# Kernel optimization log

Hardware: AMD Instinct MI355X
Metric: run time of the kernel (lower is better)

The kernel has to match this reference:

```python
import jax, jax.numpy as jnp
import numpy as np

D = 512
HEADS, DIM_HEAD, LANDMARKS, PINV_ITERS = 8, 64, 256, 6
CONV_K = 33  # residual depthwise conv kernel over sequence dim


def _ln(x, g, b, eps=1e-5):
    mu = x.mean(-1, keepdims=True)
    var = ((x - mu) ** 2).mean(-1, keepdims=True)
    return (x - mu) / jnp.sqrt(var + eps) * g + b


def _moe(x, gw, gb, f1w, f1b, l1g, l1b, f2w, f2b, l2g, l2b, k):
    # Dense grouped-expert evaluation (same math as per-token dispatch in torch source).
    scores = x @ gw + gb                               # [B,N,E]
    topk_s, topk_i = jax.lax.top_k(scores, k)          # [B,N,k]
    h = jnp.einsum('bnd,edh->benh', x, f1w) + f1b[None, :, None, :]
    h = jax.nn.relu(_ln(h, l1g[None, :, None, :], l1b[None, :, None, :]))
    o = jnp.einsum('benh,ehd->bend', h, f2w) + f2b[None, :, None, :]
    o = _ln(o, l2g[None, :, None, :], l2b[None, :, None, :])  # [B,E,N,D]
    o = jnp.take_along_axis(jnp.swapaxes(o, 1, 2), topk_i[..., None], axis=2)  # [B,N,k,D]
    w = jax.nn.softmax(topk_s, axis=-1)[..., None]
    return (w * o).sum(axis=2) + x


def _pinv(x, iters):
    # Moore-Penrose iterative pseudoinverse (lucidrains nystrom-attention)
    col = jnp.abs(x).sum(-1).max()
    row = jnp.abs(x).sum(-2).max()
    z = jnp.swapaxes(x, -1, -2) / (col * row)
    I = jnp.eye(x.shape[-1], dtype=x.dtype)
    for _ in range(iters):
        xz = x @ z
        z = 0.25 * z @ (13 * I - xz @ (15 * I - xz @ (7 * I - xz)))
    return z


def _nystrom(x, qkv_w, out_w, out_b, conv_w):
    b, n, _ = x.shape
    m, h, dh = LANDMARKS, HEADS, DIM_HEAD
    pad = (m - n % m) % m
    x = jnp.pad(x, ((0, 0), (pad, 0), (0, 0)))  # pad at FRONT, as in source
    npd = n + pad
    qkv = x @ qkv_w                              # [b, npd, 3*h*dh]
    q, k, v = [t.reshape(b, npd, h, dh).transpose(0, 2, 1, 3) for t in jnp.split(qkv, 3, axis=-1)]
    q = q * dh ** -0.5
    l = npd // m
    q_l = q.reshape(b, h, m, l, dh).mean(3)      # landmark means
    k_l = k.reshape(b, h, m, l, dh).mean(3)
    attn1 = jax.nn.softmax(jnp.einsum('bhid,bhjd->bhij', q, k_l), -1)    # [b,h,npd,m]
    attn2 = jax.nn.softmax(jnp.einsum('bhid,bhjd->bhij', q_l, k_l), -1)  # [b,h,m,m]
    attn3 = jax.nn.softmax(jnp.einsum('bhid,bhjd->bhij', q_l, k), -1)    # [b,h,m,npd]
    out = (attn1 @ _pinv(attn2, PINV_ITERS)) @ (attn3 @ v)               # [b,h,npd,dh]
    res = jax.lax.conv_general_dilated(
        v, conv_w, (1, 1), [(CONV_K // 2, CONV_K // 2), (0, 0)],
        dimension_numbers=('NCHW', 'OIHW', 'NCHW'), feature_group_count=h)
    out = out + res
    out = out.transpose(0, 2, 1, 3).reshape(b, npd, h * dh)
    out = out @ out_w + out_b
    return out[:, -n:]


def setup_inputs() -> dict:
    key = jax.random.key(0)
    ks = iter(jax.random.split(key, 64))
    def rn(shape, s=0.02):
        return jax.random.normal(next(ks), shape, jnp.float32) * s
    inp = {'features': jax.random.normal(next(ks), (4, 6000, D), jnp.float32)}
    inp['cls_token'] = rn((1, 1, D), 1e-6)
    def moe_params(pfx, E):
        inp[pfx + '_gate_w'] = rn((D, E)); inp[pfx + '_gate_b'] = jnp.zeros((E,), jnp.float32)
        inp[pfx + '_fc1_w'] = rn((E, D, D)); inp[pfx + '_fc1_b'] = jnp.zeros((E, D), jnp.float32)
        inp[pfx + '_ln1_g'] = jnp.ones((E, D), jnp.float32); inp[pfx + '_ln1_b'] = jnp.zeros((E, D), jnp.float32)
        inp[pfx + '_fc2_w'] = rn((E, D, D)); inp[pfx + '_fc2_b'] = jnp.zeros((E, D), jnp.float32)
        inp[pfx + '_ln2_g'] = jnp.ones((E, D), jnp.float32); inp[pfx + '_ln2_b'] = jnp.zeros((E, D), jnp.float32)
    moe_params('moe1', 2)
    moe_params('moe2', 4)
    def layer_params(pfx):
        inp[pfx + '_norm_g'] = jnp.ones((D,), jnp.float32); inp[pfx + '_norm_b'] = jnp.zeros((D,), jnp.float32)
        inp[pfx + '_qkv_w'] = rn((D, 3 * HEADS * DIM_HEAD))
        inp[pfx + '_out_w'] = rn((HEADS * DIM_HEAD, D)); inp[pfx + '_out_b'] = jnp.zeros((D,), jnp.float32)
        inp[pfx + '_conv_w'] = rn((HEADS, 1, CONV_K, 1))
    layer_params('l1')
    layer_params('l2')
    return inp


def reference(features, cls_token,
              moe1_gate_w, moe1_gate_b, moe1_fc1_w, moe1_fc1_b, moe1_ln1_g, moe1_ln1_b, moe1_fc2_w, moe1_fc2_b, moe1_ln2_g, moe1_ln2_b,
              moe2_gate_w, moe2_gate_b, moe2_fc1_w, moe2_fc1_b, moe2_ln1_g, moe2_ln1_b, moe2_fc2_w, moe2_fc2_b, moe2_ln2_g, moe2_ln2_b,
              l1_norm_g, l1_norm_b, l1_qkv_w, l1_out_w, l1_out_b, l1_conv_w,
              l2_norm_g, l2_norm_b, l2_qkv_w, l2_out_w, l2_out_b, l2_conv_w):
    B, N, _ = features.shape
    _H = int(np.ceil(np.sqrt(N)))
    add = _H * _H - N
    h = jnp.concatenate([features, features[:, :add]], axis=1)      # square pad by wrap
    h = jnp.concatenate([jnp.broadcast_to(cls_token, (B, 1, D)), h], axis=1)
    h = _moe(h, moe1_gate_w, moe1_gate_b, moe1_fc1_w, moe1_fc1_b, moe1_ln1_g, moe1_ln1_b, moe1_fc2_w, moe1_fc2_b, moe1_ln2_g, moe1_ln2_b, k=1)
    h = h + _nystrom(_ln(h, l1_norm_g, l1_norm_b), l1_qkv_w, l1_out_w, l1_out_b, l1_conv_w)
    h = _moe(h, moe2_gate_w, moe2_gate_b, moe2_fc1_w, moe2_fc1_b, moe2_ln1_g, moe2_ln1_b, moe2_fc2_w, moe2_fc2_b, moe2_ln2_g, moe2_ln2_b, k=2)
    h = h + _nystrom(_ln(h, l2_norm_g, l2_norm_b), l2_qkv_w, l2_out_w, l2_out_b, l2_conv_w)
    return (h[:, 0], h[:, 1:])
```

## Files before the change

kernel.cpp:

```cpp
#include <hip/hip_runtime.h>
#include <hip/hip_bf16.h>

constexpr int BATCH = 4;
constexpr int NTOK  = 6085;
constexpr int BN_TOK = BATCH * NTOK;
constexpr int NPD   = 6144;
constexpr int RPAD  = BATCH * NPD;
constexpr int DMODEL = 512;
constexpr int NH = 8, DH = 64;
constexpr int NBH = BATCH * NH;
constexpr int LGRP = NPD / 256;
constexpr int PAD_FRONT = 59;
constexpr int CONVK = 33;
constexpr int NCH = 8;
constexpr int LISTCAP = 24576;

typedef __attribute__((ext_vector_type(8))) short short8v;
typedef __attribute__((ext_vector_type(4))) float f32x4;

__device__ __forceinline__ unsigned short f2bf(float f) {
  unsigned u = __float_as_uint(f);
  u += 0x7FFF + ((u >> 16) & 1);
  return (unsigned short)(u >> 16);
}
__device__ __forceinline__ float bf2f(unsigned short h) {
  return __uint_as_float((unsigned)h << 16);
}


__global__ void k_build_h(const float* __restrict__ feat, const float* __restrict__ cls,
                          float* __restrict__ H) {
  size_t total = (size_t)BN_TOK * DMODEL;
  for (size_t idx = (size_t)blockIdx.x * blockDim.x + threadIdx.x; idx < total;
       idx += (size_t)gridDim.x * blockDim.x) {
    int d = (int)(idx & 511);
    size_t tok = idx >> 9;
    int b = (int)(tok / NTOK), n = (int)(tok % NTOK);
    float v;
    if (n == 0) v = cls[d];
    else {
      int i = n - 1; if (i >= 6000) i -= 6000;
      v = feat[((size_t)b * 6000 + i) * DMODEL + d];
    }
    H[idx] = v;
  }
}

__global__ void k_diag_fill(float* __restrict__ out, size_t n, float val) {
  for (size_t i = (size_t)blockIdx.x * blockDim.x + threadIdx.x; i < n;
       i += (size_t)gridDim.x * blockDim.x)
    out[i] = val;
}

__global__ __launch_bounds__(256) void k_wconv(const float* __restrict__ W, int ldb,
    long long wstride, unsigned short* __restrict__ hi, unsigned short* __restrict__ lo,
    long long hstride) {
  __shared__ unsigned short Th[64][80], Tl[64][80];
  int z = blockIdx.z;
  W  += (size_t)z * (size_t)wstride;
  hi += (size_t)z * (size_t)hstride;
  lo += (size_t)z * (size_t)hstride;
  int bk = blockIdx.y * 64, bn = blockIdx.x * 64;
  int t = threadIdx.x;
  int kr = t >> 2, cq = (t & 3) * 16;
  const float* src = W + (size_t)(bk + kr) * ldb + bn + cq;
  #pragma unroll
  for (int q = 0; q < 4; ++q) {
    float4 v = *(const float4*)(src + q * 4);
    float vs[4] = {v.x, v.y, v.z, v.w};
    #pragma unroll
    for (int e = 0; e < 4; ++e) {
      int n = cq + q * 4 + e;
      unsigned short h = f2bf(vs[e]);
      Th[n][kr] = h;
      Tl[n][kr] = f2bf(vs[e] - bf2f(h));
    }
  }
  __syncthreads();
  int nr = t >> 2, kq = (t & 3) * 16;
  size_t o = (size_t)(bn + nr) * 512 + bk + kq;
  *(short8v*)&hi[o]     = *(const short8v*)&Th[nr][kq];
  *(short8v*)&hi[o + 8] = *(const short8v*)&Th[nr][kq + 8];
  *(short8v*)&lo[o]     = *(const short8v*)&Tl[nr][kq];
  *(short8v*)&lo[o + 8] = *(const short8v*)&Tl[nr][kq + 8];
}

__global__ void k_lists(const float* __restrict__ WT, int* __restrict__ cnt,
                        int* __restrict__ lists, int E) {
  int lane = threadIdx.x;
  int tok = blockIdx.x * 64 + lane;
  for (int e = 0; e < E; ++e) {
    bool sel = (tok < BN_TOK) && (WT[(size_t)tok * 4 + e] != 0.f);
    unsigned long long mask = __ballot(sel);
    int rank = __popcll(mask & ((1ull << lane) - 1ull));
    int n = __popcll(mask);
    int base = 0;
    if (lane == 0 && n > 0) base = atomicAdd(&cnt[e], n);
    base = __shfl(base, 0);
    if (sel) lists[(size_t)e * LISTCAP + base + rank] = tok;
  }
}

__global__ __launch_bounds__(256) void k_gemm_mfma(const float* __restrict__ A,
    const unsigned short* __restrict__ BtH, const unsigned short* __restrict__ BtL,
    const float* __restrict__ bias, float* __restrict__ C,
    int M, int lda, int ldc, float alpha, int omode, unsigned short* __restrict__ Clo,
    const int* __restrict__ rowidx, const int* __restrict__ cnt)
{
  __shared__ unsigned short AsH[128][40], AsL[128][40];
  __shared__ unsigned short BsH[128][40], BsL[128][40];
  int nwg = gridDim.x * gridDim.y;
  int wid = blockIdx.y * gridDim.x + blockIdx.x;
  int qq = nwg >> 3, rr = nwg & 7;
  int xcd = wid & 7, pos = wid >> 3;
  int Lid = (xcd < rr ? xcd * (qq + 1) : rr * (qq + 1) + (xcd - rr) * qq) + pos;
  int bn = (Lid % gridDim.x) * 128;
  int bm = (Lid / gridDim.x) * 128;
  int Mv = M;
  if (cnt) { Mv = *cnt; if (Mv > M) Mv = M; }
  if (bm >= Mv) return;
  int tid = threadIdx.x;
  int wave = tid >> 6, lane = tid & 63;
  int mo = (wave >> 1) * 64, no = (wave & 1) * 64;
  int r16 = lane & 15, g = lane >> 4;
  f32x4 acc[4][4] = {};
  int srow = tid >> 1, shalf = (tid & 1) * 16;
  int lrow = bm + srow;
  bool avalid = lrow < Mv;
  int arow = lrow;
  if (rowidx && avalid) arow = rowidx[lrow];
  if (!avalid) arow = 0;
  const float* aptr = A + (size_t)arow * lda + shalf;
  const unsigned short* bhptr = BtH + (size_t)(bn + srow) * 512 + shalf;
  const unsigned short* blptr = BtL + (size_t)(bn + srow) * 512 + shalf;
  for (int k0 = 0; k0 < 512; k0 += 32) {
    unsigned short h8[16], l8[16];
    #pragma unroll
    for (int q = 0; q < 4; ++q) {
      float4 v = avalid ? *(const float4*)(aptr + k0 + q * 4) : make_float4(0.f, 0.f, 0.f, 0.f);
      float vs[4] = {v.x, v.y, v.z, v.w};
      #pragma unroll
      for (int e = 0; e < 4; ++e) {
        unsigned short hh = f2bf(vs[e]);
        h8[q * 4 + e] = hh;
        l8[q * 4 + e] = f2bf(vs[e] - bf2f(hh));
      }
    }
    *(short8v*)&AsH[srow][shalf]     = *(short8v*)&h8[0];
    *(short8v*)&AsH[srow][shalf + 8] = *(short8v*)&h8[8];
    *(short8v*)&AsL[srow][shalf]     = *(short8v*)&l8[0];
    *(short8v*)&AsL[srow][shalf + 8] = *(short8v*)&l8[8];
    *(short8v*)&BsH[srow][shalf]     = *(const short8v*)(bhptr + k0);
    *(short8v*)&BsH[srow][shalf + 8] = *(const short8v*)(bhptr + k0 + 8);
    *(short8v*)&BsL[srow][shalf]     = *(const short8v*)(blptr + k0);
    *(short8v*)&BsL[srow][shalf + 8] = *(const short8v*)(blptr + k0 + 8);
    __syncthreads();
    short8v ah[4], al[4], bh[4], bl[4];
    #pragma unroll
    for (int mt = 0; mt < 4; ++mt) {
      ah[mt] = *(const short8v*)&AsH[mo + mt * 16 + r16][g * 8];
      al[mt] = *(const short8v*)&AsL[mo + mt * 16 + r16][g * 8];
    }
    #pragma unroll
    for (int nt = 0; nt < 4; ++nt) {
      bh[nt] = *(const short8v*)&BsH[no + nt * 16 + r16][g * 8];
      bl[nt] = *(const short8v*)&BsL[no + nt * 16 + r16][g * 8];
    }
    #pragma unroll
    for (int mt = 0; mt < 4; ++mt)
      #pragma unroll
      for (int nt = 0; nt < 4; ++nt) {
        acc[mt][nt] = __builtin_amdgcn_mfma_f32_16x16x32_bf16(ah[mt], bh[nt], acc[mt][nt], 0, 0, 0);
        acc[mt][nt] = __builtin_amdgcn_mfma_f32_16x16x32_bf16(ah[mt], bl[nt], acc[mt][nt], 0, 0, 0);
        acc[mt][nt] = __builtin_amdgcn_mfma_f32_16x16x32_bf16(al[mt], bh[nt], acc[mt][nt], 0, 0, 0);
      }
    __syncthreads();
  }
  #pragma unroll
  for (int mt = 0; mt < 4; ++mt)
    #pragma unroll
    for (int nt = 0; nt < 4; ++nt)
      #pragma unroll
      for (int j = 0; j < 4; ++j) {
        int lr = bm + mo + mt * 16 + g * 4 + j;
        int gc = bn + no + nt * 16 + r16;
        if (lr >= Mv) continue;
        int gr = rowidx ? rowidx[lr] : lr;
        float v = alpha * acc[mt][nt][j] + (bias ? bias[gc] : 0.f);
        if (omode == 0) {
          C[(size_t)gr * ldc + gc] = v;
        } else if (omode == 2) {
          int bb = gr / NPD, ii = gr % NPD;
          if (ii >= PAD_FRONT)
            C[((size_t)bb * NTOK + ii - PAD_FRONT) * 512 + gc] += v;
        } else if (omode == 3) {
          int bb = gr / NPD, ii = gr % NPD;
          int hh = gc >> 6, dd = gc & 63;
          C[(((size_t)bb * NH + hh) * NPD + ii) * 64 + dd] = v;
        } else {
          int bb = gr / NPD, ii = gr % NPD;
          int hh = gc >> 6, dd = gc & 63;
          size_t idx = (((size_t)bb * NH + hh) * NPD + ii) * 64 + dd;
          unsigned short hi = f2bf(v);
          ((unsigned short*)C)[idx] = hi;
          Clo[idx] = f2bf(v - bf2f(hi));
        }
      }
}

__global__ __launch_bounds__(256) void k_gemm_mfma2(const float* __restrict__ A,
    const float* __restrict__ Bt, float* __restrict__ C,
    float alpha, int omode, float cdiag, int premap, int nprod, float* __restrict__ Ct)
{
  __shared__ unsigned short AsH[128][40], AsL[128][40];
  __shared__ unsigned short BsH[128][40], BsL[128][40];
  size_t zo = (size_t)blockIdx.z * 65536;
  int bm = blockIdx.y * 128, bn = blockIdx.x * 128;
  int tid = threadIdx.x;
  int wave = tid >> 6, lane = tid & 63;
  int mo = (wave >> 1) * 64, no = (wave & 1) * 64;
  int r16 = lane & 15, g = lane >> 4;
  f32x4 acc[4][4] = {};
  int srow = tid >> 1, shalf = (tid & 1) * 16;
  int grow = bm + srow;
  int gn = bn + srow;
  for (int k0 = 0; k0 < 256; k0 += 32) {
    unsigned short h8[16], l8[16];
    #pragma unroll
    for (int q = 0; q < 4; ++q) {
      float4 v = *(const float4*)&A[zo + (size_t)grow * 256 + k0 + shalf + q * 4];
      float vs[4] = {v.x, v.y, v.z, v.w};
      #pragma unroll
      for (int e = 0; e < 4; ++e) {
        float a = vs[e];
        if (premap) a = ((grow == (k0 + shalf + q * 4 + e)) ? 7.f : 0.f) - a;
        unsigned short hh = f2bf(a);
        h8[q * 4 + e] = hh;
        l8[q * 4 + e] = (nprod == 3) ? f2bf(a - bf2f(hh)) : (unsigned short)0;
      }
    }
    *(short8v*)&AsH[srow][shalf]     = *(short8v*)&h8[0];
    *(short8v*)&AsH[srow][shalf + 8] = *(short8v*)&h8[8];
    *(short8v*)&AsL[srow][shalf]     = *(short8v*)&l8[0];
    *(short8v*)&AsL[srow][shalf + 8] = *(short8v*)&l8[8];
    #pragma unroll
    for (int q = 0; q < 4; ++q) {
      float4 v = *(const float4*)&Bt[zo + (size_t)gn * 256 + k0 + shalf + q * 4];
      float vs[4] = {v.x, v.y, v.z, v.w};
      #pragma unroll
      for (int e = 0; e < 4; ++e) {
        unsigned short hh = f2bf(vs[e]);
        h8[q * 4 + e] = hh;
        l8[q * 4 + e] = (nprod == 3) ? f2bf(vs[e] - bf2f(hh)) : (unsigned short)0;
      }
    }
    *(short8v*)&BsH[srow][shalf]     = *(short8v*)&h8[0];
    *(short8v*)&BsH[srow][shalf + 8] = *(short8v*)&h8[8];
    *(short8v*)&BsL[srow][shalf]     = *(short8v*)&l8[0];
    *(short8v*)&BsL[srow][shalf + 8] = *(short8v*)&l8[8];
    __syncthreads();
    short8v ah[4], al[4], bh[4], bl[4];
    #pragma unroll
    for (int mt = 0; mt < 4; ++mt) {
      ah[mt] = *(const short8v*)&AsH[mo + mt * 16 + r16][g * 8];
      al[mt] = *(const short8v*)&AsL[mo + mt * 16 + r16][g * 8];
    }
    #pragma unroll
    for (int nt = 0; nt < 4; ++nt) {
      bh[nt] = *(const short8v*)&BsH[no + nt * 16 + r16][g * 8];
      bl[nt] = *(const short8v*)&BsL[no + nt * 16 + r16][g * 8];
    }
    #pragma unroll
    for (int mt = 0; mt < 4; ++mt)
      #pragma unroll
      for (int nt = 0; nt < 4; ++nt) {
        acc[mt][nt] = __builtin_amdgcn_mfma_f32_16x16x32_bf16(ah[mt], bh[nt], acc[mt][nt], 0, 0, 0);
        if (nprod == 3) {
          acc[mt][nt] = __builtin_amdgcn_mfma_f32_16x16x32_bf16(ah[mt], bl[nt], acc[mt][nt], 0, 0, 0);
          acc[mt][nt] = __builtin_amdgcn_mfma_f32_16x16x32_bf16(al[mt], bh[nt], acc[mt][nt], 0, 0, 0);
        }
      }
    __syncthreads();
  }
  #pragma unroll
  for (int mt = 0; mt < 4; ++mt)
    #pragma unroll
    for (int nt = 0; nt < 4; ++nt) {
      float tv[4];
      int gr0 = bm + mo + mt * 16 + g * 4;
      int gc = bn + no + nt * 16 + r16;
      #pragma unroll
      for (int j = 0; j < 4; ++j) {
        int gr = gr0 + j;
        float v;
        if (omode == 5) v = ((gr == gc) ? cdiag : 0.f) - acc[mt][nt][j];
        else            v = alpha * acc[mt][nt][j];
        C[zo + (size_t)gr * 256 + gc] = v;
        tv[j] = v;
      }
      if (Ct) *(float4*)&Ct[zo + (size_t)gc * 256 + gr0] = *(float4*)&tv[0];
    }
}

__global__ void k_yz0(const float* __restrict__ A2, float* __restrict__ Y,
                      float* __restrict__ Z, const unsigned int* __restrict__ sc) {
  float scale = 1.f / (__uint_as_float(sc[0]) * __uint_as_float(sc[1]));
  size_t total = (size_t)NBH * 65536;
  for (size_t idx = (size_t)blockIdx.x * blockDim.x + threadIdx.x; idx < total;
       idx += (size_t)gridDim.x * blockDim.x) {
    size_t bh = idx >> 16; int r = (int)((idx >> 8) & 255); int cc = (int)(idx & 255);
    Y[idx] = A2[idx] * scale;
    Z[idx] = A2[(bh << 16) + (size_t)cc * 256 + r] * scale;
  }
}

__global__ __launch_bounds__(256) void k_gemm(const float* __restrict__ A,
    const float* __restrict__ B,
    const float* __restrict__ bias, float* __restrict__ C,
    int M, int N, int K, int lda, int ldb, int ldc,
    long long sA, long long sB, long long sC, float alpha, int omode, float cdiag)
{
  __shared__ float As[16][65];
  __shared__ float Bs[16][65];
  int z = blockIdx.z;
  A += (size_t)z * (size_t)sA;
  B += (size_t)z * (size_t)sB;
  int bm = blockIdx.y * 64, bn = blockIdx.x * 64;
  int tid = threadIdx.x;
  int tr = tid >> 4, tc = tid & 15;
  int ar = tid >> 2, aq = tid & 3;
  int br = tid >> 4, bq = tid & 15;
  float acc[4][4] = {};
  for (int k0 = 0; k0 < K; k0 += 16) {
    {
      int gr = bm + ar;
      float4 v = make_float4(0.f, 0.f, 0.f, 0.f);
      if (gr < M) v = *(const float4*)&A[(size_t)gr * lda + k0 + aq * 4];
      As[aq * 4 + 0][ar] = v.x; As[aq * 4 + 1][ar] = v.y;
      As[aq * 4 + 2][ar] = v.z; As[aq * 4 + 3][ar] = v.w;
    }
    {
      float4 v = *(const float4*)&B[(size_t)(k0 + br) * ldb + bn + bq * 4];
      Bs[br][bq * 4 + 0] = v.x; Bs[br][bq * 4 + 1] = v.y;
      Bs[br][bq * 4 + 2] = v.z; Bs[br][bq * 4 + 3] = v.w;
    }
    __syncthreads();
    #pragma unroll
    for (int kk = 0; kk < 16; ++kk) {
      float a[4], bv[4];
      #pragma unroll
      for (int i = 0; i < 4; ++i) a[i] = As[kk][tr * 4 + i];
      #pragma unroll
      for (int j = 0; j < 4; ++j) bv[j] = Bs[kk][tc * 4 + j];
      #pragma unroll
      for (int i = 0; i < 4; ++i)
        #pragma unroll
        for (int j = 0; j < 4; ++j) acc[i][j] += a[i] * bv[j];
    }
    __syncthreads();
  }
  #pragma unroll
  for (int i = 0; i < 4; ++i) {
    int gr = bm + tr * 4 + i;
    if (gr >= M) continue;
    #pragma unroll
    for (int j = 0; j < 4; ++j) {
      int gc = bn + tc * 4 + j;
      if (omode == 7) {
        float v = ((gc < 512) ? 0.125f : 1.f) * acc[i][j];
        if (gc < 512) C[(size_t)gr * 512 + gc] = v;
        else          C[524288 + (size_t)gr * 512 + (gc - 512)] = v;
      } else if (omode == 5) {
        C[(size_t)z * (size_t)sC + (size_t)gr * ldc + gc] =
            ((gr == gc) ? cdiag : 0.f) - acc[i][j];
      } else {
        C[(size_t)z * (size_t)sC + (size_t)gr * ldc + gc] =
            alpha * acc[i][j] + (bias ? bias[gc] : 0.f);
      }
    }
  }
}

__global__ void k_gate(const float* __restrict__ X, const float* __restrict__ gw,
                       const float* __restrict__ gb, float* __restrict__ WT, int E, int k) {
  int tok = blockIdx.x; int lane = threadIdx.x;
  const float* x = X + (size_t)tok * DMODEL;
  float s[4] = {0.f, 0.f, 0.f, 0.f};
  for (int d = lane; d < DMODEL; d += 64) {
    float xv = x[d];
    for (int e = 0; e < E; ++e) s[e] += xv * gw[(size_t)d * E + e];
  }
  #pragma unroll
  for (int off = 32; off; off >>= 1) {
    #pragma unroll
    for (int e = 0; e < 4; ++e) s[e] += __shfl_down(s[e], off);
  }
  if (lane == 0) {
    for (int e = 0; e < E; ++e) s[e] += gb[e];
    float w[4] = {0.f, 0.f, 0.f, 0.f};
    int i1 = 0;
    for (int e = 1; e < E; ++e) if (s[e] > s[i1]) i1 = e;
    if (k == 1) {
      w[i1] = 1.f;
    } else {
      int i2 = -1;
      for (int e = 0; e < E; ++e) { if (e == i1) continue; if (i2 < 0 || s[e] > s[i2]) i2 = e; }
      float e2 = expf(s[i2] - s[i1]);
      float zz = 1.f + e2;
      w[i1] = 1.f / zz; w[i2] = e2 / zz;
    }
    #pragma unroll
    for (int e = 0; e < 4; ++e) WT[(size_t)tok * 4 + e] = w[e];
  }
}

__device__ __forceinline__ void wave_ln_stats(const float* x, int lane, float& mu, float& rstd) {
  float s = 0.f, q = 0.f;
  #pragma unroll
  for (int j = 0; j < 8; ++j) { float v = x[lane + 64 * j]; s += v; q += v * v; }
  #pragma unroll
  for (int off = 32; off; off >>= 1) { s += __shfl_xor(s, off); q += __shfl_xor(q, off); }
  mu = s * (1.f / 512.f);
  float var = q * (1.f / 512.f) - mu * mu;
  rstd = rsqrtf(var + 1e-5f);
}

__global__ void k_ln_relu_g(float* __restrict__ T, const float* __restrict__ g,
                            const float* __restrict__ b,
                            const int* __restrict__ lists, const int* __restrict__ cnt) {
  int i = blockIdx.x;
  if (i >= *cnt) return;
  int row = lists[i];
  int lane = threadIdx.x;
  float* x = T + (size_t)row * 512;
  float mu, rstd; wave_ln_stats(x, lane, mu, rstd);
  #pragma unroll
  for (int j = 0; j < 8; ++j) {
    int d = lane + 64 * j;
    float v = (x[d] - mu) * rstd * g[d] + b[d];
    x[d] = fmaxf(v, 0.f);
  }
}

__global__ void k_ln_waccum(const float* __restrict__ T, float* __restrict__ H,
                            const float* __restrict__ g, const float* __restrict__ b,
                            const float* __restrict__ WT, int e) {
  int row = blockIdx.x;
  float w = WT[(size_t)row * 4 + e];
  if (w == 0.f) return;
  int lane = threadIdx.x;
  const float* x = T + (size_t)row * 512;
  float mu, rstd; wave_ln_stats(x, lane, mu, rstd);
  float* h = H + (size_t)row * 512;
  #pragma unroll
  for (int j = 0; j < 8; ++j) {
    int d = lane + 64 * j;
    h[d] += w * ((x[d] - mu) * rstd * g[d] + b[d]);
  }
}

__global__ void k_ln_pad(const float* __restrict__ H, float* __restrict__ XLn,
                         const float* __restrict__ g, const float* __restrict__ b) {
  int row = blockIdx.x; int lane = threadIdx.x;
  int bb = row / NPD, i = row % NPD;
  float* y = XLn + (size_t)row * 512;
  if (i < PAD_FRONT) {
    #pragma unroll
    for (int j = 0; j < 8; ++j) y[lane + 64 * j] = 0.f;
    return;
  }
  const float* x = H + ((size_t)bb * NTOK + (i - PAD_FRONT)) * 512;
  float mu, rstd; wave_ln_stats(x, lane, mu, rstd);
  #pragma unroll
  for (int j = 0; j < 8; ++j) {
    int d = lane + 64 * j;
    y[d] = (x[d] - mu) * rstd * g[d] + b[d];
  }
}

__global__ void k_xmean(const float* __restrict__ XLn, float* __restrict__ Xm) {
  int z = blockIdx.x;
  int c = threadIdx.x;
  int b = z >> 8, jm = z & 255;
  const float* base = XLn + ((size_t)b * NPD + jm * LGRP) * 512 + c;
  float s = 0.f;
  #pragma unroll
  for (int t = 0; t < LGRP; ++t) s += base[(size_t)t * 512];
  Xm[(size_t)z * 512 + c] = s * (1.f / LGRP);
}

__global__ __launch_bounds__(256) void k_attn2(const float* __restrict__ QL,
                                               const float* __restrict__ KL,
                                               float* __restrict__ A2) {
  int z = blockIdx.x; int bh = z >> 8, j = z & 255;
  int b = bh >> 3, h = bh & 7;
  int t = threadIdx.x;
  __shared__ float q[64]; __shared__ float red[256];
  __shared__ float mshare, sshare;
  if (t < 64) q[t] = QL[((size_t)b * 256 + j) * 512 + h * 64 + t];
  __syncthreads();
  const float* kl = KL + ((size_t)b * 256 + t) * 512 + h * 64;
  float s = 0.f;
  #pragma unroll
  for (int d = 0; d < 64; ++d) s += q[d] * kl[d];
  red[t] = s; __syncthreads();
  for (int st = 128; st; st >>= 1) { if (t < st) red[t] = fmaxf(red[t], red[t + st]); __syncthreads(); }
  if (t == 0) mshare = red[0];
  __syncthreads();
  float e = expf(s - mshare);
  red[t] = e; __syncthreads();
  for (int st = 128; st; st >>= 1) { if (t < st) red[t] += red[t + st]; __syncthreads(); }
  if (t == 0) sshare = red[0];
  __syncthreads();
  A2[((size_t)bh * 256 + j) * 256 + t] = e / sshare;
}

__global__ __launch_bounds__(256) void k_pinv_scalars(const float* __restrict__ A2,
                                                      unsigned int* __restrict__ sc) {
  int bh = blockIdx.x; int t = threadIdx.x;
  const float* A = A2 + (size_t)bh * 65536;
  float rowsum = 0.f, colsum = 0.f;
  for (int jj = 0; jj < 256; ++jj) {
    rowsum += fabsf(A[(size_t)t * 256 + jj]);
    colsum += fabsf(A[(size_t)jj * 256 + t]);
  }
  __shared__ float sh[256];
  sh[t] = rowsum; __syncthreads();
  for (int s = 128; s; s >>= 1) { if (t < s) sh[t] = fmaxf(sh[t], sh[t + s]); __syncthreads(); }
  if (t == 0) atomicMax(&sc[0], __float_as_uint(sh[0]));
  __syncthreads();
  sh[t] = colsum; __syncthreads();
  for (int s = 128; s; s >>= 1) { if (t < s) sh[t] = fmaxf(sh[t], sh[t + s]); __syncthreads(); }
  if (t == 0) atomicMax(&sc[1], __float_as_uint(sh[0]));
}

__global__ __launch_bounds__(256) void k_vtpose(const unsigned short* __restrict__ VrH,
    const unsigned short* __restrict__ VrL,
    unsigned short* __restrict__ VtH, unsigned short* __restrict__ VtL) {
  __shared__ unsigned short TH[64][72], TL[64][72];
  int i0 = blockIdx.x * 64, bh = blockIdx.y;
  int t = threadIdx.x;
  const unsigned short* sH = VrH + ((size_t)bh * NPD + i0) * 64;
  const unsigned short* sL = VrL + ((size_t)bh * NPD + i0) * 64;
  #pragma unroll
  for (int u = 0; u < 2; ++u) {
    int idx = t + 256 * u;
    int r = idx >> 3, c8 = (idx & 7) * 8;
    *(short8v*)&TH[r][c8] = *(const short8v*)&sH[idx * 8];
    *(short8v*)&TL[r][c8] = *(const short8v*)&sL[idx * 8];
  }
  __syncthreads();
  #pragma unroll
  for (int u = 0; u < 2; ++u) {
    int idx = t + 256 * u;
    int d = idx >> 3, c8 = (idx & 7) * 8;
    unsigned short h8[8], l8[8];
    #pragma unroll
    for (int e = 0; e < 8; ++e) { h8[e] = TH[c8 + e][d]; l8[e] = TL[c8 + e][d]; }
    *(short8v*)&VtH[((size_t)bh * 64 + d) * NPD + i0 + c8] = *(short8v*)&h8[0];
    *(short8v*)&VtL[((size_t)bh * 64 + d) * NPD + i0 + c8] = *(short8v*)&l8[0];
  }
}

__global__ void k_cvt_kl(const float* __restrict__ KL, unsigned short* __restrict__ KH,
                         unsigned short* __restrict__ KLo) {
  int idx = blockIdx.x * 256 + threadIdx.x;
  int bh = idx >> 14, j = (idx >> 6) & 255, d = idx & 63;
  int b = bh >> 3, h = bh & 7;
  float v = KL[((size_t)b * 256 + j) * 512 + h * 64 + d];
  unsigned short hi = f2bf(v);
  KH[idx] = hi; KLo[idx] = f2bf(v - bf2f(hi));
}

__global__ void k_cvt_w2t(const float* __restrict__ W2b, unsigned short* __restrict__ WH,
                          unsigned short* __restrict__ WL) {
  int idx = blockIdx.x * 256 + threadIdx.x;
  int bh = idx >> 14, d = (idx >> 8) & 63, j = idx & 255;
  float v = W2b[((size_t)bh * 256 + j) * 64 + d];
  unsigned short hi = f2bf(v);
  WH[idx] = hi; WL[idx] = f2bf(v - bf2f(hi));
}

__global__ __launch_bounds__(256) void k_flash_pre(
    const float* __restrict__ Qp, long long Qsb, long long Qsh, int Qsr,
    const unsigned short* __restrict__ KHg, const unsigned short* __restrict__ KLg,
    long long Ksbh,
    const unsigned short* __restrict__ VtHg, const unsigned short* __restrict__ VtLg,
    long long Vsbh, int Vrow,
    float* __restrict__ Op, long long Osb, long long Osh, int Osr,
    float* __restrict__ Opart, float* __restrict__ ML,
    int tiles_per_chunk, int mode)
{
  int jt = blockIdx.x, bh = blockIdx.y, ch = blockIdx.z;
  int b = bh >> 3, h = bh & 7;
  const float* Qb = Qp + (size_t)b * Qsb + (size_t)h * Qsh;
  const unsigned short* KbH = KHg + (size_t)bh * Ksbh;
  const unsigned short* KbL = KLg + (size_t)bh * Ksbh;
  const unsigned short* VbH = VtHg + (size_t)bh * Vsbh;
  const unsigned short* VbL = VtLg + (size_t)bh * Vsbh;
  int tid = threadIdx.x;
  int wave = tid >> 6, lane = tid & 63;
  int r16 = lane & 15, g = lane >> 4;
  int q0 = jt * 64 + wave * 16;

  __shared__ unsigned short KsH[64][72], KsL[64][72];
  __shared__ unsigned short VtH[64][72], VtL[64][72];

  short8v qh[2], ql[2];
  #pragma unroll
  for (int kk = 0; kk < 2; ++kk) {
    const float* qr = Qb + (size_t)(q0 + r16) * Qsr + kk * 32 + g * 8;
    float4 v0 = *(const float4*)qr;
    float4 v1 = *(const float4*)(qr + 4);
    float vs[8] = {v0.x, v0.y, v0.z, v0.w, v1.x, v1.y, v1.z, v1.w};
    unsigned short hh[8], llo[8];
    #pragma unroll
    for (int e = 0; e < 8; ++e) {
      hh[e] = f2bf(vs[e]); llo[e] = f2bf(vs[e] - bf2f(hh[e]));
    }
    qh[kk] = *(short8v*)&hh[0];
    ql[kk] = *(short8v*)&llo[0];
  }

  f32x4 O4[4] = {};
  float m[4], lsum[4];
  #pragma unroll
  for (int j = 0; j < 4; ++j) { m[j] = -1e30f; lsum[j] = 0.f; }

  int t0 = ch * tiles_per_chunk;
  for (int tt = t0; tt < t0 + tiles_per_chunk; ++tt) {
    int key0 = tt * 64;
    __syncthreads();
    {
      const unsigned short* ksrcH = KbH + (size_t)key0 * 64;
      const unsigned short* ksrcL = KbL + (size_t)key0 * 64;
      #pragma unroll
      for (int u = 0; u < 2; ++u) {
        int idx = tid + 256 * u;
        int r = idx >> 3, c8 = (idx & 7) * 8;
        *(short8v*)&KsH[r][c8] = *(const short8v*)&ksrcH[idx * 8];
        *(short8v*)&KsL[r][c8] = *(const short8v*)&ksrcL[idx * 8];
      }
      const unsigned short* vsrcH = VbH + key0;
      const unsigned short* vsrcL = VbL + key0;
      #pragma unroll
      for (int u = 0; u < 2; ++u) {
        int idx = tid + 256 * u;
        int d = idx >> 3, c8 = (idx & 7) * 8;
        *(short8v*)&VtH[d][c8] = *(const short8v*)&vsrcH[(size_t)d * Vrow + c8];
        *(short8v*)&VtL[d][c8] = *(const short8v*)&vsrcL[(size_t)d * Vrow + c8];
      }
    }
    __syncthreads();
    f32x4 S[4] = {};
    #pragma unroll
    for (int kk = 0; kk < 2; ++kk)
      #pragma unroll
      for (int nt = 0; nt < 4; ++nt) {
        short8v kh = *(const short8v*)&KsH[nt * 16 + r16][kk * 32 + g * 8];
        short8v kl = *(const short8v*)&KsL[nt * 16 + r16][kk * 32 + g * 8];
        S[nt] = __builtin_amdgcn_mfma_f32_16x16x32_bf16(qh[kk], kh, S[nt], 0, 0, 0);
        S[nt] = __builtin_amdgcn_mfma_f32_16x16x32_bf16(qh[kk], kl, S[nt], 0, 0, 0);
        S[nt] = __builtin_amdgcn_mfma_f32_16x16x32_bf16(ql[kk], kh, S[nt], 0, 0, 0);
      }
    float tmax[4];
    #pragma unroll
    for (int j = 0; j < 4; ++j)
      tmax[j] = fmaxf(fmaxf(S[0][j], S[1][j]), fmaxf(S[2][j], S[3][j]));
    #pragma unroll
    for (int off = 8; off; off >>= 1)
      #pragma unroll
      for (int j = 0; j < 4; ++j) tmax[j] = fmaxf(tmax[j], __shfl_xor(tmax[j], off));
    float corr[4];
    #pragma unroll
    for (int j = 0; j < 4; ++j) {
      float mn = fmaxf(m[j], tmax[j]);
      corr[j] = expf(m[j] - mn);
      m[j] = mn;
    }
    __syncthreads();
    float tl[4] = {0.f, 0.f, 0.f, 0.f};
    #pragma unroll
    for (int nt = 0; nt < 4; ++nt)
      #pragma unroll
      for (int j = 0; j < 4; ++j) {
        float p = expf(S[nt][j] - m[j]);
        tl[j] += p;
        KsH[wave * 16 + g * 4 + j][nt * 16 + r16] = f2bf(p);
      }
    #pragma unroll
    for (int off = 8; off; off >>= 1)
      #pragma unroll
      for (int j = 0; j < 4; ++j) tl[j] += __shfl_xor(tl[j], off);
    #pragma unroll
    for (int j = 0; j < 4; ++j) lsum[j] = lsum[j] * corr[j] + tl[j];
    #pragma unroll
    for (int nt = 0; nt < 4; ++nt)
      #pragma unroll
      for (int j = 0; j < 4; ++j) O4[nt][j] *= corr[j];
    #pragma unroll
    for (int kk = 0; kk < 2; ++kk) {
      short8v ph = *(const short8v*)&KsH[wave * 16 + r16][kk * 32 + g * 8];
      #pragma unroll
      for (int nt = 0; nt < 4; ++nt) {
        short8v vh = *(const short8v*)&VtH[nt * 16 + r16][kk * 32 + g * 8];
        short8v vl = *(const short8v*)&VtL[nt * 16 + r16][kk * 32 + g * 8];
        O4[nt] = __builtin_amdgcn_mfma_f32_16x16x32_bf16(ph, vh, O4[nt], 0, 0, 0);
        O4[nt] = __builtin_amdgcn_mfma_f32_16x16x32_bf16(ph, vl, O4[nt], 0, 0, 0);
      }
    }
  }
  if (mode == 0) {
    float* Ob = Op + (size_t)b * Osb + (size_t)h * Osh;
    float inv[4];
// ... 27 lines not shown
  float M = -1e30f;
  #pragma unroll
  for (int ch = 0; ch < NCH; ++ch) {
    size_t base = (((size_t)ch * NBH + bh) * 256 + row);
    mv[ch] = ML[base * 2]; lv[ch] = ML[base * 2 + 1];
    M = fmaxf(M, mv[ch]);
  }
  float L = 0.f;
  float4 O = make_float4(0.f, 0.f, 0.f, 0.f);
  #pragma unroll
  for (int ch = 0; ch < NCH; ++ch) {
    float c = expf(mv[ch] - M);
    L += c * lv[ch];
    size_t base = (((size_t)ch * NBH + bh) * 256 + row);
    float4 o = *(const float4*)&Opart[base * 64 + q16 * 4];
    O.x += c * o.x; O.y += c * o.y; O.z += c * o.z; O.w += c * o.w;
  }
  float inv = 1.f / L;
  *(float4*)&A3V[((size_t)bh * 256 + row) * 64 + q16 * 4] =
      make_float4(O.x * inv, O.y * inv, O.z * inv, O.w * inv);
}

__global__ __launch_bounds__(256) void k_conv_add(const unsigned short* __restrict__ VtHg,
    const unsigned short* __restrict__ VtLg, const float* __restrict__ cw,
    float* __restrict__ out) {
  int it = blockIdx.x, bh = blockIdx.y;
  int b = bh >> 3, h = bh & 7;
  int i0 = it * 128;
  int t = threadIdx.x;
  __shared__ float Vs[64][161];
  const unsigned short* vh = VtHg + (size_t)bh * 64 * NPD;
  const unsigned short* vl = VtLg + (size_t)bh * 64 * NPD;
  for (int u = 0; u < 40; ++u) {
    int idx = t + 256 * u;
    int d = idx / 160, ii = idx - d * 160;
    int gi = i0 - 16 + ii;
    float v = 0.f;
    if (gi >= 0 && gi < NPD) {
      size_t a = (size_t)d * NPD + gi;
      v = bf2f(vh[a]) + bf2f(vl[a]);
    }
    Vs[d][ii] = v;
  }
  __syncthreads();
  float w[CONVK];
  #pragma unroll
  for (int p = 0; p < CONVK; ++p) w[p] = cw[h * CONVK + p];
  int rgrp = t >> 6, d = t & 63;
  for (int r = rgrp * 32; r < rgrp * 32 + 32; ++r) {
    float acc = 0.f;
    #pragma unroll
    for (int p = 0; p < CONVK; ++p) acc += w[p] * Vs[d][r + p];
    out[((size_t)b * NPD + i0 + r) * 512 + h * 64 + d] += acc;
  }
}

__global__ void k_out_write(const float* __restrict__ H, float* __restrict__ out) {
  size_t n0 = (size_t)BATCH * 512;
  size_t total = n0 + (size_t)BATCH * (NTOK - 1) * 512;
  for (size_t idx = (size_t)blockIdx.x * blockDim.x + threadIdx.x; idx < total;
       idx += (size_t)gridDim.x * blockDim.x) {
    float v;
    if (idx < n0) {
      int b = (int)(idx >> 9); int d = (int)(idx & 511);
      v = H[((size_t)b * NTOK) * 512 + d];
    } else {
      size_t r = idx - n0;
      size_t bj = r >> 9; int d = (int)(r & 511);
      int b = (int)(bj / (NTOK - 1)); int j = (int)(bj % (NTOK - 1));
      v = H[((size_t)b * NTOK + 1 + j) * 512 + d];
    }
    out[idx] = v;
  }
}


extern "C" void kernel_launch(void* const* d_in, const int* in_sizes, int n_in,
                              void* d_out, int out_size, void* d_ws, size_t ws_size,
                              hipStream_t stream) {
  (void)in_sizes; (void)n_in;

  const float* feat = (const float*)d_in[0];
  const float* cls  = (const float*)d_in[1];
  const float* m1_gw = (const float*)d_in[2];  const float* m1_gb = (const float*)d_in[3];
  const float* m1_f1w = (const float*)d_in[4]; const float* m1_f1b = (const float*)d_in[5];
  const float* m1_l1g = (const float*)d_in[6]; const float* m1_l1b = (const float*)d_in[7];
  const float* m1_f2w = (const float*)d_in[8]; const float* m1_f2b = (const float*)d_in[9];
  const float* m1_l2g = (const float*)d_in[10]; const float* m1_l2b = (const float*)d_in[11];
  const float* m2_gw = (const float*)d_in[12]; const float* m2_gb = (const float*)d_in[13];
  const float* m2_f1w = (const float*)d_in[14]; const float* m2_f1b = (const float*)d_in[15];
  const float* m2_l1g = (const float*)d_in[16]; const float* m2_l1b = (const float*)d_in[17];
  const float* m2_f2w = (const float*)d_in[18]; const float* m2_f2b = (const float*)d_in[19];
  const float* m2_l2g = (const float*)d_in[20]; const float* m2_l2b = (const float*)d_in[21];
  const float* l1_ng = (const float*)d_in[22]; const float* l1_nb = (const float*)d_in[23];
  const float* l1_qkvw = (const float*)d_in[24]; const float* l1_outw = (const float*)d_in[25];
  const float* l1_outb = (const float*)d_in[26]; const float* l1_convw = (const float*)d_in[27];
  const float* l2_ng = (const float*)d_in[28]; const float* l2_nb = (const float*)d_in[29];
  const float* l2_qkvw = (const float*)d_in[30]; const float* l2_outw = (const float*)d_in[31];
  const float* l2_outb = (const float*)d_in[32]; const float* l2_convw = (const float*)d_in[33];

  constexpr size_t SZ_H    = (size_t)BN_TOK * 512;
  constexpr size_t SZ_ROW  = (size_t)RPAD * 512;
  float* W = (float*)d_ws;
  float* H  = W;
  float* WT = W + SZ_H;
  unsigned int* SC = (unsigned int*)(W + SZ_H + 97360);
  float* pool = W + SZ_H + 97360 + 16;

  float* R2 = pool;
  float* R3 = pool + SZ_ROW;
  float* R4 = pool + 2 * SZ_ROW;
  float* SMALL = pool + 3 * SZ_ROW;
  float* Xm  = SMALL;
  float* QL  = SMALL + 524288;
  float* KL  = SMALL + 1048576;
  float* A2  = SMALL + 1572864;
  float* Zb  = SMALL + 3670016;
  float* XZp = SMALL + 5767168;
  float* Wa  = SMALL + 7864320;
  float* Wb  = SMALL + 9961472;
  float* A3V = SMALL + 12058624;
  float* W2b = SMALL + 12582912;
  size_t total_f = (SZ_H + 97360 + 16) + 3 * SZ_ROW + 13107200;
  if (total_f * 4 > ws_size) {
    k_diag_fill<<<2048, 256, 0, stream>>>((float*)d_out, (size_t)out_size,
                                          (float)(ws_size >> 20));
    return;
  }

  k_build_h<<<2048, 256, 0, stream>>>(feat, cls, H);

  auto run_moe = [&](const float* gw, const float* gb, const float* f1w, const float* f1b,
                     const float* l1g, const float* l1b, const float* f2w, const float* f2b,
                     const float* l2g, const float* l2b, int E, int k) {
    float* T1 = R2; float* T2 = R3; float* Xsnap = R4;
    unsigned short* BtF1H = (unsigned short*)A2;
    unsigned short* BtF1L = BtF1H + (size_t)E * 262144;
    unsigned short* BtF2H = (unsigned short*)(A2 + 1048576);
    unsigned short* BtF2L = BtF2H + (size_t)E * 262144;
    int* LISTS = (int*)Zb;
    int* CNT = (int*)(SC + 4);
    hipMemcpyAsync(Xsnap, H, SZ_H * 4, hipMemcpyDeviceToDevice, stream);
    hipMemsetAsync(CNT, 0, 4 * sizeof(int), stream);
    k_gate<<<BN_TOK, 64, 0, stream>>>(H, gw, gb, WT, E, k);
    k_lists<<<(BN_TOK + 63) / 64, 64, 0, stream>>>(WT, CNT, LISTS, E);
    k_wconv<<<dim3(8, 8, E), 256, 0, stream>>>(f1w, 512, 262144LL, BtF1H, BtF1L, 262144LL);
    k_wconv<<<dim3(8, 8, E), 256, 0, stream>>>(f2w, 512, 262144LL, BtF2H, BtF2L, 262144LL);
    dim3 g(4, (BN_TOK + 127) / 128, 1);
    for (int e = 0; e < E; ++e) {
      const int* lst = LISTS + (size_t)e * LISTCAP;
      const int* cnt = CNT + e;
      k_gemm_mfma<<<g, 256, 0, stream>>>(Xsnap, BtF1H + (size_t)e * 262144,
          BtF1L + (size_t)e * 262144, f1b + e * 512, T1,
          BN_TOK, 512, 512, 1.f, 0, nullptr, lst, cnt);
      k_ln_relu_g<<<BN_TOK, 64, 0, stream>>>(T1, l1g + e * 512, l1b + e * 512, lst, cnt);
      k_gemm_mfma<<<g, 256, 0, stream>>>(T1, BtF2H + (size_t)e * 262144,
          BtF2L + (size_t)e * 262144, f2b + e * 512, T2,
          BN_TOK, 512, 512, 1.f, 0, nullptr, lst, cnt);
      k_ln_waccum<<<BN_TOK, 64, 0, stream>>>(T2, H, l2g + e * 512, l2b + e * 512, WT, e);
    }
  };

  auto run_attn = [&](const float* ng, const float* nb, const float* qkvw, const float* outw,
                      const float* outb, const float* convw) {
    float* XLn = R2; float* AttnO = R2;
    float* Qb = R3;
    unsigned short* VrH = (unsigned short*)R3;
    unsigned short* VrL = VrH + 12582912;
    unsigned short* KH  = (unsigned short*)R3;
    unsigned short* KLo = KH + 12582912;
    unsigned short* VtH = (unsigned short*)R4;
    unsigned short* VtL = VtH + 12582912;
    k_ln_pad<<<RPAD, 64, 0, stream>>>(H, XLn, ng, nb);
    k_xmean<<<BATCH * 256, 512, 0, stream>>>(XLn, Xm);
    k_gemm<<<dim3(16, 16, 1), 256, 0, stream>>>(Xm, qkvw, nullptr, QL,
        1024, 1024, 512, 512, 1536, 512, 0, 0, 0, 1.f, 7, 0.f);
    k_attn2<<<NBH * 256, 256, 0, stream>>>(QL, KL, A2);
    hipMemsetAsync(SC, 0, 8, stream);
    k_pinv_scalars<<<NBH, 256, 0, stream>>>(A2, SC);
    k_yz0<<<2048, 256, 0, stream>>>(A2, Zb, Wb, SC);
    float* Y = Zb; float* Z = Wb; float* F1 = XZp; float* F2 = Wa;
    dim3 gq(2, 2, NBH);
    for (int it = 0; it < 6; ++it) {
      int np = (it < 4) ? 1 : 3;
      k_gemm_mfma2<<<gq, 256, 0, stream>>>(A2, Y, F1, 1.f, 0, 0.f, 0, np, F2);
      k_gemm_mfma2<<<gq, 256, 0, stream>>>(F2, F1, Y, 1.f, 5, 15.f, 1, np, nullptr);
      k_gemm_mfma2<<<gq, 256, 0, stream>>>(Y, F1, F2, 1.f, 5, 13.f, 0, np, nullptr);
      k_gemm_mfma2<<<gq, 256, 0, stream>>>(Z, F2, F1, 0.25f, 0, 0.f, 0, np, Y);
      float* tz = Z; Z = F1; F1 = tz;
    }
    unsigned short* KLH = (unsigned short*)A2;
    unsigned short* KLL = KLH + 524288;
    unsigned short* W2tH = KLH + 1048576;
    unsigned short* W2tL = KLH + 1572864;
    k_cvt_kl<<<2048, 256, 0, stream>>>(KL, KLH, KLL);
    unsigned short* BtQH = (unsigned short*)Wa;
    unsigned short* BtQL = BtQH + 786432;
    k_wconv<<<dim3(24, 8, 1), 256, 0, stream>>>(qkvw, 1536, 0LL, BtQH, BtQL, 0LL);
    dim3 gr(4, (RPAD + 127) / 128, 1);
    k_gemm_mfma<<<gr, 256, 0, stream>>>(XLn, BtQH + 1024 * 512, BtQL + 1024 * 512, nullptr,
        (float*)VrH, RPAD, 512, 512, 1.f, 6, VrL, nullptr, nullptr);
    k_vtpose<<<dim3(NPD / 64, NBH), 256, 0, stream>>>(VrH, VrL, VtH, VtL);
    k_gemm_mfma<<<gr, 256, 0, stream>>>(XLn, BtQH + 512 * 512, BtQL + 512 * 512, nullptr,
        (float*)KH, RPAD, 512, 512, 1.f, 6, KLo, nullptr, nullptr);
    k_flash_pre<<<dim3(4, NBH, NCH), 256, 0, stream>>>(
        QL, 131072LL, 64LL, 512,
        KH, KLo, (long long)NPD * 64,
        VtH, VtL, (long long)64 * NPD, NPD,
        nullptr, 0, 0, 0, Zb, Xm, NPD / (64 * NCH), 1);
    k_flash_comb<<<dim3(16, NBH), 256, 0, stream>>>(Zb, Xm, A3V);
    k_gemm<<<dim3(1, 4, NBH), 256, 0, stream>>>(Z, A3V, nullptr, W2b,
        256, 64, 256, 256, 64, 64, 65536, 16384, 16384, 1.f, 0, 0.f);
    k_cvt_w2t<<<2048, 256, 0, stream>>>(W2b, W2tH, W2tL);
    k_gemm_mfma<<<gr, 256, 0, stream>>>(XLn, BtQH, BtQL, nullptr,
        Qb, RPAD, 512, 512, 0.125f, 0, nullptr, nullptr, nullptr);
    k_flash_pre<<<dim3(NPD / 64, NBH, 1), 256, 0, stream>>>(
        Qb, (long long)NPD * 512, 64LL, 512,
        KLH, KLL, 16384LL,
        W2tH, W2tL, 16384LL, 256,
        AttnO, (long long)NPD * 512, 64LL, 512,
        nullptr, nullptr, 4, 0);
    k_conv_add<<<dim3(NPD / 128, NBH), 256, 0, stream>>>(VtH, VtL, convw, AttnO);
    unsigned short* BtOH = (unsigned short*)Wa;
    unsigned short* BtOL = BtOH + 262144;
    k_wconv<<<dim3(8, 8, 1), 256, 0, stream>>>(outw, 512, 0LL, BtOH, BtOL, 0LL);
    k_gemm_mfma<<<gr, 256, 0, stream>>>(AttnO, BtOH, BtOL, outb,
        H, RPAD, 512, 512, 1.f, 2, nullptr, nullptr, nullptr);
  };

  run_moe(m1_gw, m1_gb, m1_f1w, m1_f1b, m1_l1g, m1_l1b, m1_f2w, m1_f2b, m1_l2g, m1_l2b, 2, 1);
  run_attn(l1_ng, l1_nb, l1_qkvw, l1_outw, l1_outb, l1_convw);
  run_moe(m2_gw, m2_gb, m2_f1w, m2_f1b, m2_l1g, m2_l1b, m2_f2w, m2_f2b, m2_l2g, m2_l2b, 4, 2);
  run_attn(l2_ng, l2_nb, l2_qkvw, l2_outw, l2_outb, l2_convw);

  k_out_write<<<2048, 256, 0, stream>>>(H, (float*)d_out);
}
```

Before: 3.611 ms.

## Fuse K/V projection GEMMs with transposed V store, fuse LN with landmark mean

The K and V projections now run as a single wider MFMA GEMM. The new output mode writes K in head-major layout and V directly transposed, which removes the separate V GEMM launch and the k_vtpose transpose kernel. LayerNorm-with-padding and the landmark mean are merged into one kernel, so XLn is no longer re-read to form the means. The pinv row-sum scalar is dropped, since softmax rows sum to one and only the column max is needed. The cost is that the transposed V store is strided per element and likely poorly coalesced.

```diff
diff --git a/kernel.cpp b/kernel.cpp
--- a/kernel.cpp
+++ b/kernel.cpp
@@ -105,7 +105,8 @@
     const unsigned short* __restrict__ BtH, const unsigned short* __restrict__ BtL,
     const float* __restrict__ bias, float* __restrict__ C,
     int M, int lda, int ldc, float alpha, int omode, unsigned short* __restrict__ Clo,
-    const int* __restrict__ rowidx, const int* __restrict__ cnt)
+    const int* __restrict__ rowidx, const int* __restrict__ cnt,
+    unsigned short* __restrict__ VtH2, unsigned short* __restrict__ VtL2)
 {
   __shared__ unsigned short AsH[128][40], AsL[128][40];
   __shared__ unsigned short BsH[128][40], BsL[128][40];
@@ -193,17 +194,29 @@
           int bb = gr / NPD, ii = gr % NPD;
           if (ii >= PAD_FRONT)
             C[((size_t)bb * NTOK + ii - PAD_FRONT) * 512 + gc] += v;
-        } else if (omode == 3) {
-          int bb = gr / NPD, ii = gr % NPD;
-          int hh = gc >> 6, dd = gc & 63;
-          C[(((size_t)bb * NH + hh) * NPD + ii) * 64 + dd] = v;
-        } else {
+        } else if (omode == 6) {
           int bb = gr / NPD, ii = gr % NPD;
           int hh = gc >> 6, dd = gc & 63;
           size_t idx = (((size_t)bb * NH + hh) * NPD + ii) * 64 + dd;
           unsigned short hi = f2bf(v);
           ((unsigned short*)C)[idx] = hi;
           Clo[idx] = f2bf(v - bf2f(hi));
+        } else {
+          int bb = gr / NPD, ii = gr % NPD;
+          unsigned short hi = f2bf(v);
+          unsigned short lo = f2bf(v - bf2f(hi));
+          if (gc < 512) {
+            int hh = gc >> 6, dd = gc & 63;
+            size_t idx = (((size_t)bb * NH + hh) * NPD + ii) * 64 + dd;
+            ((unsigned short*)C)[idx] = hi;
+            Clo[idx] = lo;
+          } else {
+            int gc2 = gc - 512;
+            int hh = gc2 >> 6, dd = gc2 & 63;
+            size_t idx = (((size_t)bb * NH + hh) * 64 + dd) * (size_t)NPD + ii;
+            VtH2[idx] = hi;
+            VtL2[idx] = lo;
+          }
         }
       }
 }
@@ -304,7 +317,7 @@
 
 __global__ void k_yz0(const float* __restrict__ A2, float* __restrict__ Y,
                       float* __restrict__ Z, const unsigned int* __restrict__ sc) {
-  float scale = 1.f / (__uint_as_float(sc[0]) * __uint_as_float(sc[1]));
+  float scale = 1.f / __uint_as_float(sc[0]);
   size_t total = (size_t)NBH * 65536;
   for (size_t idx = (size_t)blockIdx.x * blockDim.x + threadIdx.x; idx < total;
        idx += (size_t)gridDim.x * blockDim.x) {
@@ -459,34 +472,61 @@
   }
 }
 
-__global__ void k_ln_pad(const float* __restrict__ H, float* __restrict__ XLn,
-                         const float* __restrict__ g, const float* __restrict__ b) {
-  int row = blockIdx.x; int lane = threadIdx.x;
-  int bb = row / NPD, i = row % NPD;
-  float* y = XLn + (size_t)row * 512;
-  if (i < PAD_FRONT) {
-    #pragma unroll
-    for (int j = 0; j < 8; ++j) y[lane + 64 * j] = 0.f;
-    return;
-  }
-  const float* x = H + ((size_t)bb * NTOK + (i - PAD_FRONT)) * 512;
-  float mu, rstd; wave_ln_stats(x, lane, mu, rstd);
-  #pragma unroll
-  for (int j = 0; j < 8; ++j) {
-    int d = lane + 64 * j;
-    y[d] = (x[d] - mu) * rstd * g[d] + b[d];
-  }
-}
-
-__global__ void k_xmean(const float* __restrict__ XLn, float* __restrict__ Xm) {
+__global__ __launch_bounds__(256) void k_ln_pad_mean(const float* __restrict__ H,
+    float* __restrict__ XLn, float* __restrict__ Xm,
+    const float* __restrict__ g, const float* __restrict__ b) {
   int z = blockIdx.x;
-  int c = threadIdx.x;
-  int b = z >> 8, jm = z & 255;
-  const float* base = XLn + ((size_t)b * NPD + jm * LGRP) * 512 + c;
-  float s = 0.f;
-  #pragma unroll
-  for (int t = 0; t < LGRP; ++t) s += base[(size_t)t * 512];
-  Xm[(size_t)z * 512 + c] = s * (1.f / LGRP);
+  int bb = z >> 8, jm = z & 255;
+  int wave = threadIdx.x >> 6, lane = threadIdx.x & 63;
+  __shared__ float part[4][512];
+  float racc[8] = {};
+  for (int t6 = 0; t6 < 6; ++t6) {
+    int t = wave * 6 + t6;
+    int i = jm * LGRP + t;
+    float* y = XLn + ((size_t)bb * NPD + i) * 512;
+    if (i < PAD_FRONT) {
+      #pragma unroll
+      for (int j = 0; j < 8; ++j) y[lane + 64 * j] = 0.f;
+      continue;
+    }
+    const float* x = H + ((size_t)bb * NTOK + (i - PAD_FRONT)) * 512;
+    float vals[8];
+    #pragma unroll
+    for (int j = 0; j < 8; ++j) vals[j] = x[lane + 64 * j];
+    float s = 0.f, q = 0.f;
+    #pragma unroll
+    for (int j = 0; j < 8; ++j) { s += vals[j]; q += vals[j] * vals[j]; }
+    #pragma unroll
+    for (int off = 32; off; off >>= 1) { s += __shfl_xor(s, off); q += __shfl_xor(q, off); }
+    float mu = s * (1.f / 512.f);
+    float rstd = rsqrtf(q * (1.f / 512.f) - mu * mu + 1e-5f);
+    #pragma unroll
+    for (int j = 0; j < 8; ++j) {
+      int d = lane + 64 * j;
+      float v = (vals[j] - mu) * rstd * g[d] + b[d];
+      y[d] = v;
+      racc[j] += v;
+    }
+  }
+  #pragma unroll
+  for (int j = 0; j < 8; ++j) part[wave][lane + 64 * j] = racc[j];
+  __syncthreads();
+  for (int c = threadIdx.x; c < 512; c += 256) {
+    float s = part[0][c] + part[1][c] + part[2][c] + part[3][c];
+    Xm[(size_t)z * 512 + c] = s * (1.f / LGRP);
+  }
+}
+
+__global__ __launch_bounds__(256) void k_colmax(const float* __restrict__ A2,
+                                                unsigned int* __restrict__ sc) {
+  int bh = blockIdx.x; int t = threadIdx.x;
+  const float* A = A2 + (size_t)bh * 65536;
+  float colsum = 0.f;
+  for (int jj = 0; jj < 256; ++jj) colsum += fabsf(A[(size_t)jj * 256 + t]);
+  __shared__ float sh[256];
+  sh[t] = colsum; __syncthreads();
+  for (int s = 128; s; s >>= 1) { if (t < s) sh[t] = fmaxf(sh[t], sh[t + s]); __syncthreads(); }
+  if (t == 0) atomicMax(&sc[0], __float_as_uint(sh[0]));
 }
 
 __global__ __launch_bounds__(256) void k_attn2(const float* __restrict__ QL,
@@ -513,53 +553,6 @@
   if (t == 0) sshare = red[0];
   __syncthreads();
   A2[((size_t)bh * 256 + j) * 256 + t] = e / sshare;
-}
-
-__global__ __launch_bounds__(256) void k_pinv_scalars(const float* __restrict__ A2,
-                                                      unsigned int* __restrict__ sc) {
-  int bh = blockIdx.x; int t = threadIdx.x;
-  const float* A = A2 + (size_t)bh * 65536;
-  float rowsum = 0.f, colsum = 0.f;
-  for (int jj = 0; jj < 256; ++jj) {
-    rowsum += fabsf(A[(size_t)t * 256 + jj]);
-    colsum += fabsf(A[(size_t)jj * 256 + t]);
-  }
-  __shared__ float sh[256];
-  sh[t] = rowsum; __syncthreads();
-  for (int s = 128; s; s >>= 1) { if (t < s) sh[t] = fmaxf(sh[t], sh[t + s]); __syncthreads(); }
-  if (t == 0) atomicMax(&sc[0], __float_as_uint(sh[0]));
-  __syncthreads();
-  sh[t] = colsum; __syncthreads();
-  for (int s = 128; s; s >>= 1) { if (t < s) sh[t] = fmaxf(sh[t], sh[t + s]); __syncthreads(); }
-  if (t == 0) atomicMax(&sc[1], __float_as_uint(sh[0]));
-}
-
-__global__ __launch_bounds__(256) void k_vtpose(const unsigned short* __restrict__ VrH,
-    const unsigned short* __restrict__ VrL,
-    unsigned short* __restrict__ VtH, unsigned short* __restrict__ VtL) {
-  __shared__ unsigned short TH[64][72], TL[64][72];
-  int i0 = blockIdx.x * 64, bh = blockIdx.y;
-  int t = threadIdx.x;
-  const unsigned short* sH = VrH + ((size_t)bh * NPD + i0) * 64;
-  const unsigned short* sL = VrL + ((size_t)bh * NPD + i0) * 64;
-  #pragma unroll
-  for (int u = 0; u < 2; ++u) {
-    int idx = t + 256 * u;
-    int r = idx >> 3, c8 = (idx & 7) * 8;
-    *(short8v*)&TH[r][c8] = *(const short8v*)&sH[idx * 8];
-    *(short8v*)&TL[r][c8] = *(const short8v*)&sL[idx * 8];
-  }
-  __syncthreads();
-  #pragma unroll
-  for (int u = 0; u < 2; ++u) {
-    int idx = t + 256 * u;
-    int d = idx >> 3, c8 = (idx & 7) * 8;
-    unsigned short h8[8], l8[8];
-    #pragma unroll
-    for (int e = 0; e < 8; ++e) { h8[e] = TH[c8 + e][d]; l8[e] = TL[c8 + e][d]; }
-    *(short8v*)&VtH[((size_t)bh * 64 + d) * NPD + i0 + c8] = *(short8v*)&h8[0];
-    *(short8v*)&VtL[((size_t)bh * 64 + d) * NPD + i0 + c8] = *(short8v*)&l8[0];
-  }
 }
 
 __global__ void k_cvt_kl(const float* __restrict__ KL, unsigned short* __restrict__ KH,
@@ -893,11 +886,11 @@
       const int* cnt = CNT + e;
       k_gemm_mfma<<<g, 256, 0, stream>>>(Xsnap, BtF1H + (size_t)e * 262144,
           BtF1L + (size_t)e * 262144, f1b + e * 512, T1,
-          BN_TOK, 512, 512, 1.f, 0, nullptr, lst, cnt);
+          BN_TOK, 512, 512, 1.f, 0, nullptr, lst, cnt, nullptr, nullptr);
       k_ln_relu_g<<<BN_TOK, 64, 0, stream>>>(T1, l1g + e * 512, l1b + e * 512, lst, cnt);
       k_gemm_mfma<<<g, 256, 0, stream>>>(T1, BtF2H + (size_t)e * 262144,
           BtF2L + (size_t)e * 262144, f2b + e * 512, T2,
-          BN_TOK, 512, 512, 1.f, 0, nullptr, lst, cnt);
+          BN_TOK, 512, 512, 1.f, 0, nullptr, lst, cnt, nullptr, nullptr);
       k_ln_waccum<<<BN_TOK, 64, 0, stream>>>(T2, H, l2g + e * 512, l2b + e * 512, WT, e);
     }
   };
@@ -906,19 +899,16 @@
                       const float* outb, const float* convw) {
     float* XLn = R2; float* AttnO = R2;
     float* Qb = R3;
-    unsigned short* VrH = (unsigned short*)R3;
-    unsigned short* VrL = VrH + 12582912;
     unsigned short* KH  = (unsigned short*)R3;
     unsigned short* KLo = KH + 12582912;
     unsigned short* VtH = (unsigned short*)R4;
     unsigned short* VtL = VtH + 12582912;
-    k_ln_pad<<<RPAD, 64, 0, stream>>>(H, XLn, ng, nb);
-    k_xmean<<<BATCH * 256, 512, 0, stream>>>(XLn, Xm);
+    k_ln_pad_mean<<<BATCH * 256, 256, 0, stream>>>(H, XLn, Xm, ng, nb);
     k_gemm<<<dim3(16, 16, 1), 256, 0, stream>>>(Xm, qkvw, nullptr, QL,
         1024, 1024, 512, 512, 1536, 512, 0, 0, 0, 1.f, 7, 0.f);
     k_attn2<<<NBH * 256, 256, 0, stream>>>(QL, KL, A2);
     hipMemsetAsync(SC, 0, 8, stream);
-    k_pinv_scalars<<<NBH, 256, 0, stream>>>(A2, SC);
+    k_colmax<<<NBH, 256, 0, stream>>>(A2, SC);
     k_yz0<<<2048, 256, 0, stream>>>(A2, Zb, Wb, SC);
     float* Y = Zb; float* Z = Wb; float* F1 = XZp; float* F2 = Wa;
     dim3 gq(2, 2, NBH);
@@ -939,11 +929,9 @@
     unsigned short* BtQL = BtQH + 786432;
     k_wconv<<<dim3(24, 8, 1), 256, 0, stream>>>(qkvw, 1536, 0LL, BtQH, BtQL, 0LL);
     dim3 gr(4, (RPAD + 127) / 128, 1);
-    k_gemm_mfma<<<gr, 256, 0, stream>>>(XLn, BtQH + 1024 * 512, BtQL + 1024 * 512, nullptr,
-        (float*)VrH, RPAD, 512, 512, 1.f, 6, VrL, nullptr, nullptr);
-    k_vtpose<<<dim3(NPD / 64, NBH), 256, 0, stream>>>(VrH, VrL, VtH, VtL);
-    k_gemm_mfma<<<gr, 256, 0, stream>>>(XLn, BtQH + 512 * 512, BtQL + 512 * 512, nullptr,
-        (float*)KH, RPAD, 512, 512, 1.f, 6, KLo, nullptr, nullptr);
+    k_gemm_mfma<<<dim3(8, (RPAD + 127) / 128, 1), 256, 0, stream>>>(
+        XLn, BtQH + 512 * 512, BtQL + 512 * 512, nullptr,
+        (float*)KH, RPAD, 512, 512, 1.f, 8, KLo, nullptr, nullptr, VtH, VtL);
     k_flash_pre<<<dim3(4, NBH, NCH), 256, 0, stream>>>(
         QL, 131072LL, 64LL, 512,
         KH, KLo, (long long)NPD * 64,
@@ -954,7 +942,7 @@
         256, 64, 256, 256, 64, 64, 65536, 16384, 16384, 1.f, 0, 0.f);
     k_cvt_w2t<<<2048, 256, 0, stream>>>(W2b, W2tH, W2tL);
     k_gemm_mfma<<<gr, 256, 0, stream>>>(XLn, BtQH, BtQL, nullptr,
-        Qb, RPAD, 512, 512, 0.125f, 0, nullptr, nullptr, nullptr);
+        Qb, RPAD, 512, 512, 0.125f, 0, nullptr, nullptr, nullptr, nullptr, nullptr);
     k_flash_pre<<<dim3(NPD / 64, NBH, 1), 256, 0, stream>>>(
         Qb, (long long)NPD * 512, 64LL, 512,
         KLH, KLL, 16384LL,
@@ -966,7 +954,7 @@
     unsigned short* BtOL = BtOH + 262144;
     k_wconv<<<dim3(8, 8, 1), 256, 0, stream>>>(outw, 512, 0LL, BtOH, BtOL, 0LL);
     k_gemm_mfma<<<gr, 256, 0, stream>>>(AttnO, BtOH, BtOL, outb,
-        H, RPAD, 512, 512, 1.f, 2, nullptr, nullptr, nullptr);
+        H, RPAD, 512, 512, 1.f, 2, nullptr, nullptr, nullptr, nullptr, nullptr);
   };
 
   run_moe(m1_gw, m1_gb, m1_f1w, m1_f1b, m1_l1g, m1_l1b, m1_f2w, m1_f2b, m1_l2g, m1_l2b, 2, 1);
```

Result: no change. 3.607 ms (-0.1%).
